# Kernel tuning notes

Hardware: AMD Instinct MI355X
Metric: run time of the kernel (lower is better)

The kernel has to match this reference:

```python
import jax, jax.numpy as jnp
import numpy as np

B, D_IN, D_H = 8192, 1024, 1024


def setup_inputs() -> dict:
    key = jax.random.key(0)
    k = jax.random.split(key, 7)
    s_h = 1.0 / np.sqrt(D_H)
    s_x = 1.0 / np.sqrt(D_IN)
    return {
        "x": jax.random.normal(k[0], (B, D_IN), jnp.float32),
        "h": jax.random.normal(k[1], (B, D_H), jnp.float32),
        "c": jax.random.normal(k[2], (B, D_H), jnp.float32),
        "Wh_w": jax.random.uniform(k[3], (D_H, D_H), jnp.float32, -s_h, s_h),
        "Wh_b": jax.random.uniform(k[4], (D_H,), jnp.float32, -s_h, s_h),
        "Wx_w": jax.random.uniform(k[5], (D_H, D_IN), jnp.float32, -s_x, s_x),
        "Wx_b": jax.random.uniform(k[6], (D_H,), jnp.float32, -s_x, s_x),
    }


def reference(x, h, c, Wh_w, Wh_b, Wx_w, Wx_b):
    # Source reuses the same Wh/Wx for all four gates, so the pre-activation
    # z is identical across gates: i = f = o = sigmoid(z), g = tanh(z).
    z = h @ Wh_w.T + Wh_b + x @ Wx_w.T + Wx_b  # [B, D_H]
    s = jax.nn.sigmoid(z)                      # i = f = o
    g = jnp.tanh(z)
    c_new = s * c + s * g
    h_new = s * jnp.tanh(c_new)
    return (h_new, c_new)
```

## Files before the change

kernel.cpp:

```cpp
#include <hip/hip_runtime.h>
#include <stdint.h>
#include <stddef.h>


typedef __attribute__((ext_vector_type(8))) short bf16x8;
typedef __attribute__((ext_vector_type(4))) float f32x4;
typedef __attribute__((ext_vector_type(8))) unsigned short ushort8;

#define BATCH 8192
#define DH    1024
#define KTOT  2048
#define NKT   32
#define ASLOT 16384
#define BSLOT 8192
#define LDS_BYTES ((3*ASLOT + 3*BSLOT) * 2)

__device__ __forceinline__ unsigned short f2bf(float f) {
    unsigned int u = __float_as_uint(f);
    u += 0x7FFFu + ((u >> 16) & 1u);
    return (unsigned short)(u >> 16);
}

__device__ __forceinline__ float tanh_fast(float v) {
    float a = fabsf(v);
    float e = __expf(-2.0f * a);
    float t = (1.0f - e) / (1.0f + e);
    return v < 0.0f ? -t : t;
}

__device__ __forceinline__ void gload_lds16(const void* g, void* l) {
    __builtin_amdgcn_global_load_lds(
        (const __attribute__((address_space(1))) void*)g,
        (__attribute__((address_space(3))) void*)l, 16, 0, 0);
}

#define A_CHUNKS 2097152u
#define W_CHUNKS 262144u
__global__ __launch_bounds__(256) void cast_all_kernel(
    const float* __restrict__ h, const float* __restrict__ x,
    const float* __restrict__ Whw, const float* __restrict__ Wxw,
    unsigned short* __restrict__ Abf, unsigned short* __restrict__ Wbf)
{
    for (unsigned c = blockIdx.x * 256u + threadIdx.x;
         c < A_CHUNKS + W_CHUNKS; c += gridDim.x * 256u) {
        const float* src;
        unsigned short* dst;
        if (c < A_CHUNKS) {
            unsigned base = c * 8u, r = base >> 11, k = base & 2047u;
            src = (k < 1024u) ? (h + (size_t)r * 1024u + k)
                              : (x + (size_t)r * 1024u + (k - 1024u));
            dst = Abf + base;
        } else {
            unsigned c2 = c - A_CHUNKS;
            unsigned base = c2 * 8u, r = base >> 11, k = base & 2047u;
            src = (k < 1024u) ? (Whw + (size_t)r * 1024u + k)
                              : (Wxw + (size_t)r * 1024u + (k - 1024u));
            dst = Wbf + base;
        }
        const float4* s4 = (const float4*)src;
        float4 f0 = s4[0], f1 = s4[1];
        ushort8 o;
        o[0]=f2bf(f0.x); o[1]=f2bf(f0.y); o[2]=f2bf(f0.z); o[3]=f2bf(f0.w);
        o[4]=f2bf(f1.x); o[5]=f2bf(f1.y); o[6]=f2bf(f1.z); o[7]=f2bf(f1.w);
        *(ushort8*)dst = o;
    }
}

template <int KK, int MG, bool READB, typename F>
__device__ __forceinline__ void phase_fn(
    const unsigned short* As, const unsigned short* Bs,
    int wr, int wc, int ln15, int hi, int ln7,
    f32x4 (&acc)[8][2], bf16x8 (&bfr)[2], F&& mid)
{
    bf16x8 af[4];
    #pragma unroll
    for (int i = 0; i < 4; ++i) {
        int r = wr * 128 + (MG * 4 + i) * 16 + ln15;
        af[i] = *(const bf16x8*)(As + r * 64 + (((KK * 4 + hi) ^ ln7) * 8));
    }
    if constexpr (READB) {
        #pragma unroll
        for (int n = 0; n < 2; ++n) {
            int r = wc * 32 + n * 16 + ln15;
            bfr[n] = *(const bf16x8*)(Bs + r * 64 + (((KK * 4 + hi) ^ ln7) * 8));
        }
    }
    mid();
    __builtin_amdgcn_s_barrier();
    asm volatile("s_waitcnt lgkmcnt(0)" ::: "memory");
    __builtin_amdgcn_sched_barrier(0);
    __builtin_amdgcn_s_setprio(1);
    #pragma unroll
    for (int i = 0; i < 4; ++i)
        #pragma unroll
        for (int n = 0; n < 2; ++n)
            acc[MG * 4 + i][n] = __builtin_amdgcn_mfma_f32_16x16x32_bf16(
                af[i], bfr[n], acc[MG * 4 + i][n], 0, 0, 0);
    __builtin_amdgcn_s_setprio(0);
    __builtin_amdgcn_s_barrier();
}

__global__ __launch_bounds__(512, 2) void lstm_gemm_kernel(
    const unsigned short* __restrict__ A,
    const unsigned short* __restrict__ W,
    const float* __restrict__ Whb, const float* __restrict__ Wxb,
    const float* __restrict__ Cin,
    float* __restrict__ Hout, float* __restrict__ Cout)
{
    extern __shared__ unsigned short smem[];
    unsigned short* sA = smem;
    unsigned short* sB = smem + 3 * ASLOT;

    const int tid  = threadIdx.x;
    const int wid  = tid >> 6;
    const int lane = tid & 63;
    const int wr = wid >> 2, wc = wid & 3;
    const int bidN = blockIdx.x & 7;
    const int bidM = blockIdx.x >> 3;
    const int row0 = bidM * 256, col0 = bidN * 128;
    const int ln15 = lane & 15, hi = lane >> 4, ln7 = lane & 7;

    const unsigned short* Ag = A + (size_t)row0 * KTOT;
    const unsigned short* Bg = W + (size_t)col0 * KTOT;

    f32x4 acc[8][2] = {};
    bf16x8 bfr[2];

    auto stage = [&](const unsigned short* gbase, unsigned short* lbase) {
        #pragma unroll
        for (int j = 0; j < 2; ++j) {
            int c = j * 512 + tid;
            int r = c >> 3, p = c & 7;
            const unsigned short* g = gbase + (size_t)r * KTOT + ((p ^ (r & 7)) * 8);
            unsigned short* l = lbase + (size_t)(j * 512 + wid * 64) * 8;
            gload_lds16(g, l);
        }
    };

    stage(Ag,                         sA);
    stage(Ag + (size_t)128 * KTOT,    sA + 8192);
    stage(Bg,                         sB);
    stage(Ag + 64,                    sA + ASLOT);
    stage(Ag + (size_t)128 * KTOT + 64, sA + ASLOT + 8192);
    stage(Bg + 64,                    sB + BSLOT);
    asm volatile("s_waitcnt vmcnt(6)" ::: "memory");
    __builtin_amdgcn_s_barrier();

    int scur = 0, swr = 2;
    for (int kt = 0; kt < NKT; ++kt) {
        const unsigned short* As = sA + scur * ASLOT;
        const unsigned short* Bs = sB + scur * BSLOT;
        unsigned short* Aw = sA + swr * ASLOT;
        unsigned short* Bw = sB + swr * BSLOT;
        const size_t kn = (size_t)(kt + 2) * 64;
        const bool pre = (kt < NKT - 2);

        phase_fn<0, 0, true >(As, Bs, wr, wc, ln15, hi, ln7, acc, bfr,
            [&] { if (pre) stage(Ag + kn, Aw); });
        phase_fn<0, 1, false>(As, Bs, wr, wc, ln15, hi, ln7, acc, bfr,
            [&] { if (pre) stage(Ag + (size_t)128 * KTOT + kn, Aw + 8192); });
        phase_fn<1, 0, true >(As, Bs, wr, wc, ln15, hi, ln7, acc, bfr,
            [&] { if (pre) stage(Bg + kn, Bw); });
        phase_fn<1, 1, false>(As, Bs, wr, wc, ln15, hi, ln7, acc, bfr,
            [&] {
                if (kt < NKT - 2)       asm volatile("s_waitcnt vmcnt(6)" ::: "memory");
                else if (kt == NKT - 2) asm volatile("s_waitcnt vmcnt(0)" ::: "memory");
            });

        scur = (scur == 2) ? 0 : scur + 1;
        swr  = (swr  == 2) ? 0 : swr  + 1;
    }

    const int rlo = hi * 4;
    #pragma unroll
    for (int n = 0; n < 2; ++n) {
        const int col = col0 + wc * 32 + n * 16 + ln15;
        const float bias = Whb[col] + Wxb[col];
        #pragma unroll
        for (int m = 0; m < 8; ++m) {
            #pragma unroll
            for (int j = 0; j < 4; ++j) {
                const int row = row0 + wr * 128 + m * 16 + rlo + j;
                const size_t off = (size_t)row * DH + col;
                const float z = acc[m][n][j] + bias;
                const float s = 0.5f + 0.5f * tanh_fast(0.5f * z);
                const float g = tanh_fast(z);
                const float cn = s * (Cin[off] + g);
                Hout[off] = s * tanh_fast(cn);
                Cout[off] = cn;
            }
        }
    }
}

__global__ __launch_bounds__(256) void lstm_naive_kernel(
    const float* __restrict__ x, const float* __restrict__ h,
    const float* __restrict__ c,
    const float* __restrict__ Whw, const float* __restrict__ Whb,
    const float* __restrict__ Wxw, const float* __restrict__ Wxb,
    float* __restrict__ Hout, float* __restrict__ Cout)
{
    const int idx = blockIdx.x * 256 + threadIdx.x;
    const int b = idx >> 10, n = idx & 1023;
    const float* hr = h  + (size_t)b * 1024;
    const float* xr = x  + (size_t)b * 1024;
    const float* wh = Whw + (size_t)n * 1024;
    const float* wx = Wxw + (size_t)n * 1024;
    float z = Whb[n] + Wxb[n];
    for (int k = 0; k < 1024; ++k) z += hr[k] * wh[k] + xr[k] * wx[k];
    const float s = 0.5f + 0.5f * tanh_fast(0.5f * z);
    const float g = tanh_fast(z);
    const size_t off = (size_t)b * 1024 + n;
    const float cn = s * (c[off] + g);
    Hout[off] = s * tanh_fast(cn);
    Cout[off] = cn;
}

extern "C" void kernel_launch(void* const* d_in, const int* in_sizes, int n_in,
                              void* d_out, int out_size, void* d_ws, size_t ws_size,
                              hipStream_t stream) {
    const float* x   = (const float*)d_in[0];
    const float* h   = (const float*)d_in[1];
    const float* c   = (const float*)d_in[2];
    const float* Whw = (const float*)d_in[3];
    const float* Whb = (const float*)d_in[4];
    const float* Wxw = (const float*)d_in[5];
    const float* Wxb = (const float*)d_in[6];
    float* Hout = (float*)d_out;
    float* Cout = Hout + (size_t)BATCH * DH;

    const size_t needA = (size_t)BATCH * KTOT * 2;
    const size_t needW = (size_t)DH * KTOT * 2;

    if (ws_size >= needA + needW) {
        unsigned short* Abf = (unsigned short*)d_ws;
        unsigned short* Wbf = (unsigned short*)((char*)d_ws + needA);
        cast_all_kernel<<<2304, 256, 0, stream>>>(h, x, Whw, Wxw, Abf, Wbf);
        (void)hipFuncSetAttribute((const void*)lstm_gemm_kernel,
                                  hipFuncAttributeMaxDynamicSharedMemorySize,
                                  LDS_BYTES);
        lstm_gemm_kernel<<<256, 512, LDS_BYTES, stream>>>(
            Abf, Wbf, Whb, Wxb, c, Hout, Cout);
    } else {
        lstm_naive_kernel<<<(BATCH * DH) / 256, 256, 0, stream>>>(
            x, h, c, Whw, Whb, Wxw, Wxb, Hout, Cout);
    }
}
```

Baseline: 224.4 us.

## Merge four MFMA phases into two and remap blocks for XCD locality

Each k-tile iteration now runs two phases instead of four. Each phase loads all 8 A fragments and both B fragments and issues 16 MFMAs, which halves the number of block-wide barriers per tile but raises register pressure. Separately, the block index is remapped so that consecutive blocks on the same XCD share M rows across all 8 N columns, aiming to improve L2 reuse of the A tiles. The vmcnt(6) wait now sits after the B stage in the second phase, so the wait accounting for outstanding loads changes.

```diff
diff --git a/kernel.cpp b/kernel.cpp
--- a/kernel.cpp
+++ b/kernel.cpp
@@ -66,24 +66,22 @@
     }
 }
 
-template <int KK, int MG, bool READB, typename F>
+template <int KK, typename F>
 __device__ __forceinline__ void phase_fn(
     const unsigned short* As, const unsigned short* Bs,
     int wr, int wc, int ln15, int hi, int ln7,
-    f32x4 (&acc)[8][2], bf16x8 (&bfr)[2], F&& mid)
-{
-    bf16x8 af[4];
-    #pragma unroll
-    for (int i = 0; i < 4; ++i) {
-        int r = wr * 128 + (MG * 4 + i) * 16 + ln15;
-        af[i] = *(const bf16x8*)(As + r * 64 + (((KK * 4 + hi) ^ ln7) * 8));
-    }
-    if constexpr (READB) {
-        #pragma unroll
-        for (int n = 0; n < 2; ++n) {
-            int r = wc * 32 + n * 16 + ln15;
-            bfr[n] = *(const bf16x8*)(Bs + r * 64 + (((KK * 4 + hi) ^ ln7) * 8));
-        }
+    f32x4 (&acc)[8][2], F&& mid)
+{
+    bf16x8 af[8], bfr[2];
+    #pragma unroll
+    for (int m = 0; m < 8; ++m) {
+        int r = wr * 128 + m * 16 + ln15;
+        af[m] = *(const bf16x8*)(As + r * 64 + (((KK * 4 + hi) ^ ln7) * 8));
+    }
+    #pragma unroll
+    for (int n = 0; n < 2; ++n) {
+        int r = wc * 32 + n * 16 + ln15;
+        bfr[n] = *(const bf16x8*)(Bs + r * 64 + (((KK * 4 + hi) ^ ln7) * 8));
     }
     mid();
     __builtin_amdgcn_s_barrier();
@@ -91,11 +89,11 @@
     __builtin_amdgcn_sched_barrier(0);
     __builtin_amdgcn_s_setprio(1);
     #pragma unroll
-    for (int i = 0; i < 4; ++i)
+    for (int m = 0; m < 8; ++m)
         #pragma unroll
         for (int n = 0; n < 2; ++n)
-            acc[MG * 4 + i][n] = __builtin_amdgcn_mfma_f32_16x16x32_bf16(
-                af[i], bfr[n], acc[MG * 4 + i][n], 0, 0, 0);
+            acc[m][n] = __builtin_amdgcn_mfma_f32_16x16x32_bf16(
+                af[m], bfr[n], acc[m][n], 0, 0, 0);
     __builtin_amdgcn_s_setprio(0);
     __builtin_amdgcn_s_barrier();
 }
@@ -115,8 +113,12 @@
     const int wid  = tid >> 6;
     const int lane = tid & 63;
     const int wr = wid >> 2, wc = wid & 3;
-    const int bidN = blockIdx.x & 7;
-    const int bidM = blockIdx.x >> 3;
+
+    const int orig = blockIdx.x;
+    const int xcd  = orig & 7;
+    const int loc  = orig >> 3;
+    const int bidM = xcd * 4 + (loc >> 3);
+    const int bidN = loc & 7;
     const int row0 = bidM * 256, col0 = bidN * 128;
     const int ln15 = lane & 15, hi = lane >> 4, ln7 = lane & 7;
 
@@ -124,7 +126,6 @@
     const unsigned short* Bg = W + (size_t)col0 * KTOT;
 
     f32x4 acc[8][2] = {};
-    bf16x8 bfr[2];
 
     auto stage = [&](const unsigned short* gbase, unsigned short* lbase) {
         #pragma unroll
@@ -137,12 +138,12 @@
         }
     };
 
-    stage(Ag,                         sA);
-    stage(Ag + (size_t)128 * KTOT,    sA + 8192);
-    stage(Bg,                         sB);
-    stage(Ag + 64,                    sA + ASLOT);
+    stage(Ag,                           sA);
+    stage(Ag + (size_t)128 * KTOT,      sA + 8192);
+    stage(Bg,                           sB);
+    stage(Ag + 64,                      sA + ASLOT);
     stage(Ag + (size_t)128 * KTOT + 64, sA + ASLOT + 8192);
-    stage(Bg + 64,                    sB + BSLOT);
+    stage(Bg + 64,                      sB + BSLOT);
     asm volatile("s_waitcnt vmcnt(6)" ::: "memory");
     __builtin_amdgcn_s_barrier();
 
@@ -155,17 +156,17 @@
         const size_t kn = (size_t)(kt + 2) * 64;
         const bool pre = (kt < NKT - 2);
 
-        phase_fn<0, 0, true >(As, Bs, wr, wc, ln15, hi, ln7, acc, bfr,
-            [&] { if (pre) stage(Ag + kn, Aw); });
-        phase_fn<0, 1, false>(As, Bs, wr, wc, ln15, hi, ln7, acc, bfr,
-            [&] { if (pre) stage(Ag + (size_t)128 * KTOT + kn, Aw + 8192); });
-        phase_fn<1, 0, true >(As, Bs, wr, wc, ln15, hi, ln7, acc, bfr,
-            [&] { if (pre) stage(Bg + kn, Bw); });
-        phase_fn<1, 1, false>(As, Bs, wr, wc, ln15, hi, ln7, acc, bfr,
-            [&] {
-                if (kt < NKT - 2)       asm volatile("s_waitcnt vmcnt(6)" ::: "memory");
-                else if (kt == NKT - 2) asm volatile("s_waitcnt vmcnt(0)" ::: "memory");
-            });
+        phase_fn<0>(As, Bs, wr, wc, ln15, hi, ln7, acc, [&] {
+            if (pre) {
+                stage(Ag + kn, Aw);
+                stage(Ag + (size_t)128 * KTOT + kn, Aw + 8192);
+            }
+        });
+        phase_fn<1>(As, Bs, wr, wc, ln15, hi, ln7, acc, [&] {
+            if (pre) stage(Bg + kn, Bw);
+            if (kt < NKT - 2)       asm volatile("s_waitcnt vmcnt(6)" ::: "memory");
+            else if (kt == NKT - 2) asm volatile("s_waitcnt vmcnt(0)" ::: "memory");
+        });
 
         scur = (scur == 2) ? 0 : scur + 1;
         swr  = (swr  == 2) ? 0 : swr  + 1;
```

Result: no change. 222.4 us (-0.9%).
